# Kernel tuning notes

Measured on AMD Instinct MI355X. Metric: run time of the kernel, lower is better.

## Reference

```python
import jax, jax.numpy as jnp
import numpy as np

EMBED = 1024
N_HEAD = 16
D_HID = EMBED // N_HEAD
R_FF = 4
D_FF = EMBED * R_FF
LN_EPS = 1e-5


def layer_norm(x, gamma, beta):
    mu = jnp.mean(x, axis=-1, keepdims=True)
    var = jnp.var(x, axis=-1, keepdims=True)
    return (x - mu) * jax.lax.rsqrt(var + LN_EPS) * gamma + beta


def setup_inputs() -> dict:
    key = jax.random.key(0)
    ks = jax.random.split(key, 10)
    B, S = 4, 2048
    # torch nn.Linear stores weight as [out, in]; y = x @ W.T
    def xavier(k, shape):
        fan_out, fan_in = shape
        lim = np.sqrt(6.0 / (fan_in + fan_out))
        return jax.random.uniform(k, shape, jnp.float32, -lim, lim)
    return {
        "x": jax.random.normal(ks[0], (B, S, EMBED), jnp.float32),
        "Wq": xavier(ks[1], (EMBED, EMBED)),
        "Wk": xavier(ks[2], (EMBED, EMBED)),
        "Wv": xavier(ks[3], (EMBED, EMBED)),
        "Wo": xavier(ks[4], (EMBED, EMBED)),
        "bo": jnp.zeros((EMBED,), jnp.float32),
        "ln1_g": jnp.ones((EMBED,), jnp.float32),
        "ln1_b": jnp.zeros((EMBED,), jnp.float32),
        "ln2_g": jnp.ones((EMBED,), jnp.float32),
        "ln2_b": jnp.zeros((EMBED,), jnp.float32),
        "W1": jax.random.normal(ks[5], (D_FF, EMBED), jnp.float32) * np.sqrt(2.0 / EMBED),
        "b1": jnp.zeros((D_FF,), jnp.float32),
        "W2": xavier(ks[6], (EMBED, D_FF)),
        "b2": jnp.zeros((EMBED,), jnp.float32),
    }


def reference(x, Wq, Wk, Wv, Wo, bo, ln1_g, ln1_b, ln2_g, ln2_b, W1, b1, W2, b2):
    B, S, E = x.shape
    scaling = 1.0 / np.sqrt(D_HID)
    # --- attention (pre-LN), dropout = identity (eval) ---
    xn = layer_norm(x, ln1_g, ln1_b)
    q = (xn @ Wq.T).reshape(B, S, N_HEAD, D_HID) * scaling
    k = (xn @ Wk.T).reshape(B, S, N_HEAD, D_HID)
    v = (xn @ Wv.T).reshape(B, S, N_HEAD, D_HID)
    scores = jnp.einsum("bqhd,bkhd->bhqk", q, k)
    attn = jax.nn.softmax(scores, axis=-1)
    out = jnp.einsum("bhqk,bkhd->bqhd", attn, v).reshape(B, S, E)
    out = out @ Wo.T + bo
    x = x + out
    # --- feed-forward (pre-LN) ---
    xn = layer_norm(x, ln2_g, ln2_b)
    h = jax.nn.relu(xn @ W1.T + b1)
    x = x + (h @ W2.T + b2)
    return x
```

## Files before the change

### kernel.cpp

```cpp
#include <hip/hip_runtime.h>
#include <hip/hip_bf16.h>
#include <cstdint>


typedef __attribute__((ext_vector_type(8))) short bf16x8;
typedef __attribute__((ext_vector_type(4))) float f32x4;

#define LDSAS __attribute__((address_space(3)))
#define GLBAS __attribute__((address_space(1)))

#define CQK 0.18033688011112044f

__device__ __forceinline__ unsigned short f2bf(float f) {
  union { float f; unsigned u; } c; c.f = f;
  unsigned u = c.u + 0x7fffu + ((c.u >> 16) & 1u);
  return (unsigned short)(u >> 16);
}

__device__ __forceinline__ unsigned pk2(float a, float b) {
  __hip_bfloat162 h = __float22bfloat162_rn(make_float2(a, b));
  union { __hip_bfloat162 h; unsigned u; } c; c.h = h; return c.u;
}

__device__ __forceinline__ void async16(const unsigned short* g, unsigned short* l) {
  __builtin_amdgcn_global_load_lds((const GLBAS unsigned int*)g,
                                   (LDSAS unsigned int*)l, 16, 0, 0);
}

__global__ void cvt_all(const float* __restrict__ q, const float* __restrict__ k,
                        const float* __restrict__ v, const float* __restrict__ o,
                        const float* __restrict__ w1, const float* __restrict__ w2,
                        unsigned short* __restrict__ wsb) {
  const long i = (long)blockIdx.x * 256 + threadIdx.x;
  const float* src; unsigned short* dst; long off;
  if (i < 1048576) {
    const long seg = i >> 18, o4 = i & 262143;
    src = (seg == 0) ? q : (seg == 1) ? k : (seg == 2) ? v : o;
    dst = wsb + ((seg == 3) ? 3145728L : seg * 1048576L);
    off = o4;
  } else if (i < 2097152) {
    src = w1; dst = wsb + 4194304; off = i - 1048576;
  } else {
    src = w2; dst = wsb + 8388608; off = i - 2097152;
  }
  const float4 vv = ((const float4*)src)[off];
  ushort4 r;
  r.x = f2bf(vv.x); r.y = f2bf(vv.y); r.z = f2bf(vv.z); r.w = f2bf(vv.w);
  ((ushort4*)dst)[off] = r;
}

__global__ void ln_fwd(const float* __restrict__ x, const float* __restrict__ g,
                       const float* __restrict__ bb, unsigned short* __restrict__ outp) {
  const int row = blockIdx.x, tid = threadIdx.x;
  const float4 v = ((const float4*)(x + (long)row * 1024))[tid];
  float s  = v.x + v.y + v.z + v.w;
  float sq = v.x * v.x + v.y * v.y + v.z * v.z + v.w * v.w;
#pragma unroll
  for (int off = 1; off < 64; off <<= 1) {
    s  += __shfl_xor(s, off);
    sq += __shfl_xor(sq, off);
  }
  __shared__ float red[8];
  const int wv = tid >> 6, lane = tid & 63;
  if (lane == 0) { red[wv] = s; red[4 + wv] = sq; }
  __syncthreads();
  s  = red[0] + red[1] + red[2] + red[3];
  sq = red[4] + red[5] + red[6] + red[7];
  const float mu  = s * (1.f / 1024.f);
  const float var = sq * (1.f / 1024.f) - mu * mu;
  const float rstd = rsqrtf(var + 1e-5f);
  const float4 gv = ((const float4*)g)[tid];
  const float4 bv = ((const float4*)bb)[tid];
  ushort4 o;
  o.x = f2bf((v.x - mu) * rstd * gv.x + bv.x);
  o.y = f2bf((v.y - mu) * rstd * gv.y + bv.y);
  o.z = f2bf((v.z - mu) * rstd * gv.z + bv.z);
  o.w = f2bf((v.w - mu) * rstd * gv.w + bv.w);
  ((ushort4*)(outp + (long)row * 1024))[tid] = o;
}

template <int EPI>
__launch_bounds__(256, 3)
__global__ void gemm_bt(const unsigned short* __restrict__ A,
                        const unsigned short* __restrict__ B,
                        void* __restrict__ Cout,
                        const float* __restrict__ bias,
                        const float* __restrict__ res,
                        int M, int N, int K) {
  __shared__ __align__(16) unsigned short As[128 * 64];
  __shared__ __align__(16) unsigned short Bs[128 * 64];
  const int tid  = threadIdx.x;
  const int lane = tid & 63;
  const int wvu  = __builtin_amdgcn_readfirstlane(tid >> 6);
  const int quad = lane >> 4, l16 = lane & 15;
  const int wm = wvu >> 1, wn = wvu & 1;

  const int gx = gridDim.x;
  const int id = blockIdx.y * gx + blockIdx.x;
  const int xcd = id & 7, slot = id >> 3;
  const int by = xcd * 8 + (slot & 7);
  const int bx = slot >> 3;
  const long m0 = (long)by * 128, n0 = (long)bx * 128;

  f32x4 acc[4][4];
#pragma unroll
  for (int i = 0; i < 4; i++)
#pragma unroll
    for (int j = 0; j < 4; j++) acc[i][j] = (f32x4){0.f, 0.f, 0.f, 0.f};

  const int rxA = l16 & 7;
  const int c0A = quad ^ rxA;
  int srow[4], sgc[4];
#pragma unroll
  for (int j = 0; j < 4; ++j) {
    const int s = wvu * 256 + j * 64 + lane;
    srow[j] = s >> 3;
    sgc[j] = ((s & 7) ^ (srow[j] & 7)) * 8;
  }

  for (int k0 = 0; k0 < K; k0 += 64) {
    __syncthreads();
#pragma unroll
    for (int j = 0; j < 4; ++j) {
      const int db = (wvu * 256 + j * 64) * 8;
      async16(A + (m0 + srow[j]) * K + k0 + sgc[j], As + db);
      async16(B + (n0 + srow[j]) * K + k0 + sgc[j], Bs + db);
    }
    __syncthreads();

#pragma unroll
    for (int kc = 0; kc < 2; ++kc) {
      const int ch = (c0A ^ (kc * 4)) * 8;
      bf16x8 af[4], bfr[4];
#pragma unroll
      for (int t = 0; t < 4; ++t) {
        af[t]  = *(const bf16x8*)(As + (wm * 64 + t * 16 + l16) * 64 + ch);
        bfr[t] = *(const bf16x8*)(Bs + (wn * 64 + t * 16 + l16) * 64 + ch);
      }
#pragma unroll
      for (int mt = 0; mt < 4; ++mt)
#pragma unroll
        for (int nt = 0; nt < 4; ++nt)
          acc[mt][nt] = __builtin_amdgcn_mfma_f32_16x16x32_bf16(af[mt], bfr[nt],
                                                                acc[mt][nt], 0, 0, 0);
    }
  }

#pragma unroll
  for (int nt = 0; nt < 4; ++nt) {
    const long col = n0 + wn * 64 + nt * 16 + l16;
    float bv = 0.f;
    if (EPI == 1 || EPI == 2) bv = bias[col];
    const float scl = (EPI == 3 && col < 1024) ? CQK : 1.0f;
#pragma unroll
    for (int mt = 0; mt < 4; ++mt) {
#pragma unroll
      for (int r = 0; r < 4; ++r) {
        const long row = m0 + wm * 64 + mt * 16 + quad * 4 + r;
        const long idx = row * (long)N + col;
        float v = acc[mt][nt][r];
        if (EPI == 0) {
          ((unsigned short*)Cout)[idx] = f2bf(v);
        } else if (EPI == 1) {
          ((float*)Cout)[idx] = v + bv + res[idx];
        } else if (EPI == 2) {
          v += bv;
          ((unsigned short*)Cout)[idx] = f2bf(v > 0.f ? v : 0.f);
        } else {
          ((unsigned short*)Cout)[idx] = f2bf(v * scl);
        }
      }
    }
  }
}

__global__ void vprep(const unsigned short* __restrict__ qkv,
                      unsigned short* __restrict__ vt) {
  __shared__ unsigned short T[64 * 68];
  const int tid = threadIdx.x;
  const int t = blockIdx.x;
  const int bh = blockIdx.y;
  const int b = bh >> 4, h = bh & 15;
  const long base = ((long)b * 2048 + t * 64) * 3072 + 2048 + h * 64;
#pragma unroll
  for (int i = 0; i < 4; ++i) {
    int c = i * 256 + tid;
    int r = c >> 4, d4 = (c & 15) * 4;
    *(ushort4*)(T + r * 68 + d4) = *(const ushort4*)(qkv + base + (long)r * 3072 + d4);
  }
  __syncthreads();
  unsigned short* out = vt + ((long)bh * 32 + t) * 4096;
#pragma unroll
  for (int i = 0; i < 4; ++i) {
    int u = i * 256 + tid;
    int c = u >> 1, half = u & 1;
    int d = c >> 3;
    int k = ((c & 7) - d) & 7;
    int kvp4 = k * 8 + half * 4;
    int sk = (kvp4 & 32) | ((kvp4 & 4) << 2) | ((kvp4 & 16) >> 1) | ((kvp4 & 8) >> 1);
    ushort4 o;
    o.x = T[(sk + 0) * 68 + d];
    o.y = T[(sk + 1) * 68 + d];
    o.z = T[(sk + 2) * 68 + d];
    o.w = T[(sk + 3) * 68 + d];
    *(ushort4*)(out + u * 4) = o;
  }
}

__launch_bounds__(256, 3)
__global__ void attn_fwd(const unsigned short* __restrict__ qkv,
                         const unsigned short* __restrict__ vt,
                         unsigned short* __restrict__ outp) {
  __shared__ __align__(16) unsigned short Qs[128 * 64];
  __shared__ __align__(16) unsigned short Ks[128 * 64];
  __shared__ __align__(16) unsigned short Vs[128 * 64];

  const int tid = threadIdx.x;
  const int lane = tid & 63;
  const int wv = __builtin_amdgcn_readfirstlane(tid >> 6);
  const int quad = lane >> 4, l16 = lane & 15;

  const int id = blockIdx.y * 16 + blockIdx.x;
  const int xcd = id & 7, slot = id >> 3;
  const int bh = xcd * 8 + (slot >> 4);
  const int qt = slot & 15;
  const int b = bh >> 4, h = bh & 15;
  const long rowbase = (long)b * 2048;
  const int hoff = h * 64;

  {
    const unsigned short* qsrc = qkv + (rowbase + qt * 128) * 3072 + hoff;
#pragma unroll
    for (int j = 0; j < 4; ++j) {
      const int c = j * 256 + wv * 64 + lane;
      const int row = c >> 3;
      const int k = ((c & 7) - row) & 7;
      async16(qsrc + (long)row * 3072 + k * 8, Qs + (j * 256 + wv * 64) * 8);
    }
  }
  __syncthreads();

  const int rot0 = (quad + l16) & 7;
  const int rot1 = rot0 ^ 4;

  bf16x8 bq[2][2];
#pragma unroll
  for (int s = 0; s < 2; ++s) {
    const int qrow = wv * 32 + s * 16 + l16;
    bq[s][0] = *(const bf16x8*)(Qs + qrow * 64 + rot0 * 8);
    bq[s][1] = *(const bf16x8*)(Qs + qrow * 64 + rot1 * 8);
  }

  const int c0 = wv * 64 + lane;
  const int r0 = c0 >> 3;
  const int ks = ((c0 & 7) - r0) & 7;
  const unsigned short* kptr = qkv + (rowbase + r0) * 3072 + 1024 + hoff + ks * 8;
  const unsigned short* vptr = vt + (long)bh * 131072 + (long)c0 * 8;
  unsigned short* kdst = Ks + wv * 512;
  unsigned short* vdst = Vs + wv * 512;

  bf16x8 ones;
#pragma unroll
  for (int i = 0; i < 8; ++i) ones[i] = (short)0x3F80;

  f32x4 oacc[2][4], lacc[2];
#pragma unroll
  for (int s = 0; s < 2; ++s) {
    lacc[s] = (f32x4){0.f, 0.f, 0.f, 0.f};
#pragma unroll
    for (int i = 0; i < 4; ++i) oacc[s][i] = (f32x4){0.f, 0.f, 0.f, 0.f};
  }

  for (int kt = 0; kt < 16; ++kt) {
    __syncthreads();
#pragma unroll
    for (int j = 0; j < 4; ++j) {
      async16(kptr + (long)j * 32 * 3072, kdst + j * 2048);
      async16(vptr + j * 2048, vdst + j * 2048);
    }
    kptr += (long)128 * 3072;
    vptr += 8192;
    __syncthreads();

    f32x4 sacc[2][8];
#pragma unroll
    for (int t = 0; t < 8; ++t) {
      const int ar = t * 16 + l16;
      bf16x8 ak0 = *(const bf16x8*)(Ks + ar * 64 + rot0 * 8);
      bf16x8 ak1 = *(const bf16x8*)(Ks + ar * 64 + rot1 * 8);
#pragma unroll
      for (int s = 0; s < 2; ++s) {
        f32x4 z = (f32x4){0.f, 0.f, 0.f, 0.f};
        z = __builtin_amdgcn_mfma_f32_16x16x32_bf16(ak0, bq[s][0], z, 0, 0, 0);
        sacc[s][t] = __builtin_amdgcn_mfma_f32_16x16x32_bf16(ak1, bq[s][1], z, 0, 0, 0);
      }
    }

    union APU { unsigned u[4]; bf16x8 v; } ap[2][4];
#pragma unroll
    for (int s = 0; s < 2; ++s)
#pragma unroll
      for (int hf = 0; hf < 4; ++hf) {
#pragma unroll
        for (int t = 0; t < 2; ++t) {
          const f32x4 sv = sacc[s][hf * 2 + t];
          const float p0 = __builtin_amdgcn_exp2f(sv[0]);
          const float p1 = __builtin_amdgcn_exp2f(sv[1]);
          const float p2 = __builtin_amdgcn_exp2f(sv[2]);
          const float p3 = __builtin_amdgcn_exp2f(sv[3]);
          ap[s][hf].u[t * 2 + 0] = pk2(p0, p1);
          ap[s][hf].u[t * 2 + 1] = pk2(p2, p3);
        }
        lacc[s] = __builtin_amdgcn_mfma_f32_16x16x32_bf16(ap[s][hf].v, ones,
                                                          lacc[s], 0, 0, 0);
      }

#pragma unroll
    for (int hf = 0; hf < 4; ++hf) {
      const int vbase = (hf >> 1) * 4096 + ((hf & 1) ? rot1 : rot0) * 8;
#pragma unroll
      for (int dt = 0; dt < 4; ++dt) {
        bf16x8 bv = *(const bf16x8*)(Vs + vbase + (dt * 16 + l16) * 64);
#pragma unroll
        for (int s = 0; s < 2; ++s)
          oacc[s][dt] = __builtin_amdgcn_mfma_f32_16x16x32_bf16(ap[s][hf].v, bv,
                                                                oacc[s][dt], 0, 0, 0);
      }
    }
  }

#pragma unroll
  for (int s = 0; s < 2; ++s) {
    float linv[4];
#pragma unroll
    for (int r = 0; r < 4; ++r) linv[r] = 1.f / lacc[s][r];
#pragma unroll
    for (int dt = 0; dt < 4; ++dt)
#pragma unroll
      for (int r = 0; r < 4; ++r) {
        const long row = rowbase + qt * 128 + wv * 32 + s * 16 + quad * 4 + r;
        outp[row * 1024 + hoff + dt * 16 + l16] = f2bf(oacc[s][dt][r] * linv[r]);
      }
  }
}

extern "C" void kernel_launch(void* const* d_in, const int* in_sizes, int n_in,
                              void* d_out, int out_size, void* d_ws, size_t ws_size,
                              hipStream_t stream) {
  (void)in_sizes; (void)n_in; (void)out_size; (void)ws_size;
  const float* x   = (const float*)d_in[0];
  const float* Wq  = (const float*)d_in[1];
  const float* Wk  = (const float*)d_in[2];
  const float* Wv  = (const float*)d_in[3];
  const float* Wo  = (const float*)d_in[4];
  const float* bo  = (const float*)d_in[5];
  const float* g1  = (const float*)d_in[6];
  const float* be1 = (const float*)d_in[7];
  const float* g2  = (const float*)d_in[8];
  const float* be2 = (const float*)d_in[9];
  const float* W1  = (const float*)d_in[10];
  const float* bf1 = (const float*)d_in[11];
  const float* W2  = (const float*)d_in[12];
  const float* bf2 = (const float*)d_in[13];

  char* ws = (char*)d_ws;
  unsigned short* wqkv  = (unsigned short*)(ws);
  unsigned short* wo    = (unsigned short*)(ws + 6291456);
  unsigned short* w1    = (unsigned short*)(ws + 8388608);
  unsigned short* w2    = (unsigned short*)(ws + 16777216);
  unsigned short* xn    = (unsigned short*)(ws + 25165824);
  unsigned short* big   = (unsigned short*)(ws + 41943040);
  unsigned short* attnb = (unsigned short*)(ws + 109051904);
  float*          x1    = (float*)(ws + 125829120);
  unsigned short* vtg   = xn;

  cvt_all<<<12288, 256, 0, stream>>>(Wq, Wk, Wv, Wo, W1, W2, wqkv);

  ln_fwd<<<8192, 256, 0, stream>>>(x, g1, be1, xn);
  gemm_bt<3><<<dim3(24, 64), 256, 0, stream>>>(xn, wqkv, big, nullptr, nullptr,
                                               8192, 3072, 1024);
  vprep<<<dim3(32, 64), 256, 0, stream>>>(big, vtg);
  attn_fwd<<<dim3(16, 64), 256, 0, stream>>>(big, vtg, attnb);
  gemm_bt<1><<<dim3(8, 64), 256, 0, stream>>>(attnb, wo, x1, bo, x,
                                              8192, 1024, 1024);
  ln_fwd<<<8192, 256, 0, stream>>>(x1, g2, be2, xn);
  gemm_bt<2><<<dim3(32, 64), 256, 0, stream>>>(xn, w1, big, bf1, nullptr,
                                               8192, 4096, 1024);
  gemm_bt<1><<<dim3(8, 64), 256, 0, stream>>>(big, w2, (float*)d_out, bf2, x1,
                                              8192, 1024, 4096);
}
```

Measured before the change: 458.9 us.

## Add 256x256-tile pipelined GEMM for QKV and FFN1 projections

Adds a new 512-thread GEMM kernel with 256x256 output tiles, 128 KB of dynamic LDS, double-buffered async global-to-LDS staging interleaved with MFMA phases, s_setprio scheduling hints and XCD-aware block remapping. It replaces the 128x128 gemm_bt for the QKV projection and the first FFN matmul. The larger tiles raise arithmetic intensity and cut global traffic, and the staged prefetch is meant to hide load latency behind MFMA work. In exchange, occupancy per CU is lower and the fine-grained barrier and vmcnt schedule is fragile.

```diff
diff --git a/kernel.cpp b/kernel.cpp
--- a/kernel.cpp
+++ b/kernel.cpp
@@ -164,6 +164,216 @@
         } else if (EPI == 1) {
           ((float*)Cout)[idx] = v + bv + res[idx];
         } else if (EPI == 2) {
+          v += bv;
+          ((unsigned short*)Cout)[idx] = f2bf(v > 0.f ? v : 0.f);
+        } else {
+          ((unsigned short*)Cout)[idx] = f2bf(v * scl);
+        }
+      }
+    }
+  }
+}
+
+#define LDA4(AF, BUF, H)                                                        \
+  do {                                                                          \
+    const unsigned short* _p = As + ((BUF) * 2 + (H)) * 8192;                   \
+    _Pragma("unroll") for (int _m = 0; _m < 4; ++_m) {                          \
+      AF[_m][0] = *(const bf16x8*)(_p + (_m * 32 + rA) * 64 + chk0);            \
+      AF[_m][1] = *(const bf16x8*)(_p + (_m * 32 + rA) * 64 + chk1);            \
+    }                                                                           \
+  } while (0)
+
+#define LDB2(BF, BUF, H)                                                        \
+  do {                                                                          \
+    const unsigned short* _p = Bs + ((BUF) * 2 + (H)) * 8192;                   \
+    _Pragma("unroll") for (int _n = 0; _n < 2; ++_n) {                          \
+      BF[_n][0] = *(const bf16x8*)(_p + (_n * 64 + rB) * 64 + chk0);            \
+      BF[_n][1] = *(const bf16x8*)(_p + (_n * 64 + rB) * 64 + chk1);            \
+    }                                                                           \
+  } while (0)
+
+#define MFMA8(MB, NB, AF, BF)                                                   \
+  do {                                                                          \
+    _Pragma("unroll") for (int _m = 0; _m < 4; ++_m)                            \
+    _Pragma("unroll") for (int _n = 0; _n < 2; ++_n) {                          \
+      acc[(MB) + _m][(NB) + _n] = __builtin_amdgcn_mfma_f32_16x16x32_bf16(      \
+          AF[_m][0], BF[_n][0], acc[(MB) + _m][(NB) + _n], 0, 0, 0);            \
+      acc[(MB) + _m][(NB) + _n] = __builtin_amdgcn_mfma_f32_16x16x32_bf16(      \
+          AF[_m][1], BF[_n][1], acc[(MB) + _m][(NB) + _n], 0, 0, 0);            \
+    }                                                                           \
+  } while (0)
+
+#define PH_MID()                                                                \
+  __builtin_amdgcn_s_barrier();                                                 \
+  asm volatile("s_waitcnt lgkmcnt(0)" ::: "memory");                            \
+  __builtin_amdgcn_sched_barrier(0);                                            \
+  __builtin_amdgcn_s_setprio(1)
+
+#define PH_END()                                                                \
+  __builtin_amdgcn_s_setprio(0);                                                \
+  __builtin_amdgcn_sched_barrier(0);                                            \
+  __builtin_amdgcn_s_barrier();                                                 \
+  __builtin_amdgcn_sched_barrier(0)
+
+template <int EPI>
+__launch_bounds__(512, 2)
+__global__ void gemm256(const unsigned short* __restrict__ A,
+                        const unsigned short* __restrict__ B,
+                        void* __restrict__ Cout,
+                        const float* __restrict__ bias,
+                        int M, int N, int K) {
+  extern __shared__ __align__(16) unsigned short lds[];
+  unsigned short* As = lds;
+  unsigned short* Bs = lds + 32768;
+
+  const int tid  = threadIdx.x;
+  const int lane = tid & 63;
+  const int wv   = __builtin_amdgcn_readfirstlane(tid >> 6);
+  const int quad = lane >> 4, l16 = lane & 15;
+  const int wm = wv >> 2, wn = wv & 3;
+
+  const int id = blockIdx.x;
+  const int xcd = id & 7, slot = id >> 3;
+  const int by = xcd * 4 + (slot & 3);
+  const int bx = slot >> 2;
+  const long m0 = (long)by * 256, n0 = (long)bx * 256;
+
+  const int s0 = wv * 64 + lane;
+  const int r0 = s0 >> 3;
+  const int c0 = (s0 ^ r0) & 7;
+  const int s1 = 512 + s0;
+  const int r1 = s1 >> 3;
+  const int c1 = (s1 ^ r1) & 7;
+  const long rt0 = (long)r0 * K + c0 * 8;
+  const long rt1 = (long)r1 * K + c1 * 8;
+  const unsigned short* Ab = A + m0 * K;
+  const unsigned short* Bb = B + n0 * K;
+
+  const int rA = wm * 16 + l16;
+  const int rB = wn * 16 + l16;
+  const int chk0 = (quad ^ (l16 & 7)) * 8;
+  const int chk1 = chk0 ^ 32;
+
+  f32x4 acc[8][4];
+#pragma unroll
+  for (int a_ = 0; a_ < 8; ++a_)
+#pragma unroll
+    for (int b_ = 0; b_ < 4; ++b_) acc[a_][b_] = (f32x4){0.f, 0.f, 0.f, 0.f};
+
+  auto stgA = [&](int b, int h, long kk) {
+    const unsigned short* s = Ab + (long)h * 128 * K + kk;
+    unsigned short* d = As + (b * 2 + h) * 8192 + wv * 512;
+    async16(s + rt0, d);
+    async16(s + rt1, d + 4096);
+  };
+  auto stgB = [&](int b, int h, long kk) {
+    const unsigned short* s = Bb + (long)h * 128 * K + kk;
+    unsigned short* d = Bs + (b * 2 + h) * 8192 + wv * 512;
+    async16(s + rt0, d);
+    async16(s + rt1, d + 4096);
+  };
+
+  stgA(0, 0, 0); stgA(0, 1, 0); stgB(0, 0, 0); stgB(0, 1, 0);
+  stgB(1, 0, 64); stgA(1, 0, 64); stgB(1, 1, 64);
+  asm volatile("s_waitcnt vmcnt(6)" ::: "memory");
+  __builtin_amdgcn_s_barrier();
+  __builtin_amdgcn_sched_barrier(0);
+
+  const int NI = K >> 7;
+  for (int it = 0; it < NI; ++it) {
+    const long kt  = (long)it * 128;
+    const long ku  = kt + 64;
+    const long kt2 = kt + 128;
+    const long kt3 = kt + 192;
+    const bool more = (it + 1 < NI);
+
+    bf16x8 bq[2][2];
+    {
+      bf16x8 a[4][2];
+      LDA4(a, 0, 0); LDB2(bq, 0, 0);
+      stgA(1, 1, ku);
+      PH_MID();
+      MFMA8(0, 0, a, bq);
+      PH_END();
+    }
+    {
+      bf16x8 a[4][2];
+      LDA4(a, 0, 1);
+      if (more) stgB(0, 0, kt2);
+      PH_MID();
+      MFMA8(4, 0, a, bq);
+      PH_END();
+    }
+    {
+      bf16x8 a[4][2];
+      LDA4(a, 0, 0); LDB2(bq, 0, 1);
+      PH_MID();
+      MFMA8(0, 2, a, bq);
+      PH_END();
+    }
+    {
+      bf16x8 a[4][2];
+      LDA4(a, 0, 1);
+      if (more) { stgA(0, 0, kt2); stgB(0, 1, kt2); }
+      PH_MID();
+      MFMA8(4, 2, a, bq);
+      __builtin_amdgcn_s_setprio(0);
+      __builtin_amdgcn_sched_barrier(0);
+      if (more) { asm volatile("s_waitcnt vmcnt(6)" ::: "memory"); }
+      else      { asm volatile("s_waitcnt vmcnt(0)" ::: "memory"); }
+      __builtin_amdgcn_s_barrier();
+      __builtin_amdgcn_sched_barrier(0);
+    }
+    {
+      bf16x8 a[4][2];
+      LDA4(a, 1, 0); LDB2(bq, 1, 0);
+      if (more) stgA(0, 1, kt2);
+      PH_MID();
+      MFMA8(0, 0, a, bq);
+      PH_END();
+    }
+    {
+      bf16x8 a[4][2];
+      LDA4(a, 1, 1);
+      if (more) stgB(1, 0, kt3);
+      PH_MID();
+      MFMA8(4, 0, a, bq);
+      PH_END();
+    }
+    {
+      bf16x8 a[4][2];
+      LDA4(a, 1, 0); LDB2(bq, 1, 1);
+      PH_MID();
+      MFMA8(0, 2, a, bq);
+      PH_END();
+    }
+    {
+      bf16x8 a[4][2];
+      LDA4(a, 1, 1);
+      if (more) { stgA(1, 0, kt3); stgB(1, 1, kt3); }
+      PH_MID();
+      MFMA8(4, 2, a, bq);
+      __builtin_amdgcn_s_setprio(0);
+      __builtin_amdgcn_sched_barrier(0);
+      if (more) { asm volatile("s_waitcnt vmcnt(6)" ::: "memory"); }
+      __builtin_amdgcn_s_barrier();
+      __builtin_amdgcn_sched_barrier(0);
+    }
+  }
+
+#pragma unroll
+  for (int nt = 0; nt < 4; ++nt) {
+    const long col = n0 + nt * 64 + wn * 16 + l16;
+    const float bv = (EPI == 2) ? bias[col] : 0.f;
+    const float scl = (EPI == 3 && col < 1024) ? CQK : 1.0f;
+#pragma unroll
+    for (int mt = 0; mt < 8; ++mt) {
+#pragma unroll
+      for (int r = 0; r < 4; ++r) {
+        const long row = m0 + mt * 32 + wm * 16 + quad * 4 + r;
+        const long idx = row * (long)N + col;
+        float v = acc[mt][nt][r];
+        if (EPI == 2) {
           v += bv;
           ((unsigned short*)Cout)[idx] = f2bf(v > 0.f ? v : 0.f);
         } else {
@@ -363,6 +573,15 @@
   const float* W2  = (const float*)d_in[12];
   const float* bf2 = (const float*)d_in[13];
 
+  static bool s_attr = false;
+  if (!s_attr) {
+    hipFuncSetAttribute(reinterpret_cast<const void*>(&gemm256<3>),
+                        hipFuncAttributeMaxDynamicSharedMemorySize, 131072);
+    hipFuncSetAttribute(reinterpret_cast<const void*>(&gemm256<2>),
+                        hipFuncAttributeMaxDynamicSharedMemorySize, 131072);
+    s_attr = true;
+  }
+
   char* ws = (char*)d_ws;
   unsigned short* wqkv  = (unsigned short*)(ws);
   unsigned short* wo    = (unsigned short*)(ws + 6291456);
@@ -377,15 +596,15 @@
   cvt_all<<<12288, 256, 0, stream>>>(Wq, Wk, Wv, Wo, W1, W2, wqkv);
 
   ln_fwd<<<8192, 256, 0, stream>>>(x, g1, be1, xn);
-  gemm_bt<3><<<dim3(24, 64), 256, 0, stream>>>(xn, wqkv, big, nullptr, nullptr,
-                                               8192, 3072, 1024);
+  gemm256<3><<<dim3(384), 512, 131072, stream>>>(xn, wqkv, big, nullptr,
+                                                 8192, 3072, 1024);
   vprep<<<dim3(32, 64), 256, 0, stream>>>(big, vtg);
   attn_fwd<<<dim3(16, 64), 256, 0, stream>>>(big, vtg, attnb);
   gemm_bt<1><<<dim3(8, 64), 256, 0, stream>>>(attnb, wo, x1, bo, x,
                                               8192, 1024, 1024);
   ln_fwd<<<8192, 256, 0, stream>>>(x1, g2, be2, xn);
-  gemm_bt<2><<<dim3(32, 64), 256, 0, stream>>>(xn, w1, big, bf1, nullptr,
-                                               8192, 4096, 1024);
+  gemm256<2><<<dim3(512), 512, 131072, stream>>>(xn, w1, big, bf1,
+                                                 8192, 4096, 1024);
   gemm_bt<1><<<dim3(8, 64), 256, 0, stream>>>(big, w2, (float*)d_out, bf2, x1,
                                               8192, 1024, 4096);
 }
```

After: 488.0 us. 6.3% more time.

## Double-buffer K/V tiles in attention kernel with async prefetch two tiles ahead

Applied to the files above, without the earlier changes.

Reworks the attention inner loop so K and V tiles are staged into two LDS buffers, with the load for tile kt+2 issued while tile kt is computed. Uses explicit vmcnt waits and raw barriers instead of __syncthreads, and Q is placed in the second buffer region and reused. This is meant to hide global-load latency behind MFMA work. In exchange LDS use doubles to 64KB and the occupancy hint drops from 3 to 2 blocks per CU.

```diff
diff --git a/kernel.cpp b/kernel.cpp
--- a/kernel.cpp
+++ b/kernel.cpp
@@ -207,13 +207,11 @@
   }
 }
 
-__launch_bounds__(256, 3)
+__launch_bounds__(256, 2)
 __global__ void attn_fwd(const unsigned short* __restrict__ qkv,
                          const unsigned short* __restrict__ vt,
                          unsigned short* __restrict__ outp) {
-  __shared__ __align__(16) unsigned short Qs[128 * 64];
-  __shared__ __align__(16) unsigned short Ks[128 * 64];
-  __shared__ __align__(16) unsigned short Vs[128 * 64];
+  __shared__ __align__(16) unsigned short lds[32768];
 
   const int tid = threadIdx.x;
   const int lane = tid & 63;
@@ -228,6 +226,8 @@
   const long rowbase = (long)b * 2048;
   const int hoff = h * 64;
 
+  unsigned short* Qs = lds + 16384;
+
   {
     const unsigned short* qsrc = qkv + (rowbase + qt * 128) * 3072 + hoff;
 #pragma unroll
@@ -238,7 +238,9 @@
       async16(qsrc + (long)row * 3072 + k * 8, Qs + (j * 256 + wv * 64) * 8);
     }
   }
-  __syncthreads();
+  asm volatile("s_waitcnt vmcnt(0)" ::: "memory");
+  __builtin_amdgcn_s_barrier();
+  __builtin_amdgcn_sched_barrier(0);
 
   const int rot0 = (quad + l16) & 7;
   const int rot1 = rot0 ^ 4;
@@ -250,14 +252,28 @@
     bq[s][0] = *(const bf16x8*)(Qs + qrow * 64 + rot0 * 8);
     bq[s][1] = *(const bf16x8*)(Qs + qrow * 64 + rot1 * 8);
   }
+  asm volatile("s_waitcnt lgkmcnt(0)" ::: "memory");
+  __builtin_amdgcn_sched_barrier(0);
+  __builtin_amdgcn_s_barrier();
+  __builtin_amdgcn_sched_barrier(0);
 
   const int c0 = wv * 64 + lane;
   const int r0 = c0 >> 3;
   const int ks = ((c0 & 7) - r0) & 7;
   const unsigned short* kptr = qkv + (rowbase + r0) * 3072 + 1024 + hoff + ks * 8;
   const unsigned short* vptr = vt + (long)bh * 131072 + (long)c0 * 8;
-  unsigned short* kdst = Ks + wv * 512;
-  unsigned short* vdst = Vs + wv * 512;
+
+  auto stage = [&](int t) {
+    unsigned short* kdst = lds + (t & 1) * 16384 + wv * 512;
+    unsigned short* vdst = kdst + 8192;
+    const unsigned short* kp = kptr + (long)t * 128 * 3072;
+    const unsigned short* vp = vptr + (long)t * 8192;
+#pragma unroll
+    for (int j = 0; j < 4; ++j) {
+      async16(kp + (long)j * 32 * 3072, kdst + j * 2048);
+      async16(vp + j * 2048, vdst + j * 2048);
+    }
+  };
 
   bf16x8 ones;
 #pragma unroll
@@ -271,23 +287,21 @@
     for (int i = 0; i < 4; ++i) oacc[s][i] = (f32x4){0.f, 0.f, 0.f, 0.f};
   }
 
+  stage(0); stage(1);
+  asm volatile("s_waitcnt vmcnt(8)" ::: "memory");
+  __builtin_amdgcn_s_barrier();
+  __builtin_amdgcn_sched_barrier(0);
+
   for (int kt = 0; kt < 16; ++kt) {
-    __syncthreads();
-#pragma unroll
-    for (int j = 0; j < 4; ++j) {
-      async16(kptr + (long)j * 32 * 3072, kdst + j * 2048);
-      async16(vptr + j * 2048, vdst + j * 2048);
-    }
-    kptr += (long)128 * 3072;
-    vptr += 8192;
-    __syncthreads();
+    const unsigned short* Kb = lds + (kt & 1) * 16384;
+    const unsigned short* Vb = Kb + 8192;
 
     f32x4 sacc[2][8];
 #pragma unroll
     for (int t = 0; t < 8; ++t) {
       const int ar = t * 16 + l16;
-      bf16x8 ak0 = *(const bf16x8*)(Ks + ar * 64 + rot0 * 8);
-      bf16x8 ak1 = *(const bf16x8*)(Ks + ar * 64 + rot1 * 8);
+      bf16x8 ak0 = *(const bf16x8*)(Kb + ar * 64 + rot0 * 8);
+      bf16x8 ak1 = *(const bf16x8*)(Kb + ar * 64 + rot1 * 8);
 #pragma unroll
       for (int s = 0; s < 2; ++s) {
         f32x4 z = (f32x4){0.f, 0.f, 0.f, 0.f};
@@ -320,13 +334,25 @@
       const int vbase = (hf >> 1) * 4096 + ((hf & 1) ? rot1 : rot0) * 8;
 #pragma unroll
       for (int dt = 0; dt < 4; ++dt) {
-        bf16x8 bv = *(const bf16x8*)(Vs + vbase + (dt * 16 + l16) * 64);
+        bf16x8 bv = *(const bf16x8*)(Vb + vbase + (dt * 16 + l16) * 64);
 #pragma unroll
         for (int s = 0; s < 2; ++s)
           oacc[s][dt] = __builtin_amdgcn_mfma_f32_16x16x32_bf16(ap[s][hf].v, bv,
                                                                 oacc[s][dt], 0, 0, 0);
       }
     }
+
+    if (kt == 15) break;
+    __builtin_amdgcn_s_barrier();
+    __builtin_amdgcn_sched_barrier(0);
+    if (kt + 2 < 16) {
+      stage(kt + 2);
+      asm volatile("s_waitcnt vmcnt(8)" ::: "memory");
+    } else {
+      asm volatile("s_waitcnt vmcnt(0)" ::: "memory");
+    }
+    __builtin_amdgcn_s_barrier();
+    __builtin_amdgcn_sched_barrier(0);
   }
 
 #pragma unroll
```

Measured after the change: 490.8 us. 1.07x slower.
